# Performance work log

Measured on AMD Instinct MI355X. Metric: run time of the kernel, lower is better.

Reference implementation:

```python
import jax, jax.numpy as jnp
import numpy as np

N = 400000      # total atoms
MAXD = 4        # max degree
NDEG = MAXD + 1 # degrees 0..4 (DeepChem min_degree=0)
F0 = 75         # ConvMolFeaturizer atom feature size
B = 16384       # number of graphs (batch_size)
NT = 12         # n_tasks
DIMS = [F0, 15, 20, 27, 36]


def setup_inputs() -> dict:
    key = jax.random.key(0)
    ks = jax.random.split(key, 40)
    inp = {}
    inp["atom_features"] = jax.random.normal(ks[0], (N, F0), jnp.float32)
    i = 1
    for l in range(4):
        fi, fo = DIMS[l], DIMS[l + 1]
        inp[f"Ws{l+1}"] = jax.random.normal(ks[i], (NDEG, fi, fo), jnp.float32) * 0.1; i += 1
        inp[f"Wn{l+1}"] = jax.random.normal(ks[i], (NDEG, fi, fo), jnp.float32) * 0.1; i += 1
        inp[f"b{l+1}"] = jax.random.normal(ks[i], (NDEG, fo), jnp.float32) * 0.1; i += 1
    inp["Wd2"] = jax.random.normal(ks[i], (2 * DIMS[-1], NT * 2), jnp.float32) * 0.1; i += 1
    inp["bd2"] = jnp.zeros((NT * 2,), jnp.float32)
    inp["Wl1"] = jax.random.normal(ks[i], (2 * NT, 96), jnp.float32) * 0.1; i += 1
    inp["bl1"] = jnp.zeros((96,), jnp.float32)
    inp["g1"] = jnp.ones((96,), jnp.float32)
    inp["be1"] = jnp.zeros((96,), jnp.float32)
    inp["Wl2"] = jax.random.normal(ks[i], (96, 63), jnp.float32) * 0.1; i += 1
    inp["bl2"] = jnp.zeros((63,), jnp.float32)
    inp["g2"] = jnp.ones((63,), jnp.float32)
    inp["be2"] = jnp.zeros((63,), jnp.float32)
    inp["Wl3"] = jax.random.normal(ks[i], (63, 138), jnp.float32) * 0.1; i += 1
    inp["bl3"] = jnp.zeros((138,), jnp.float32)
    inp["neighbor_list"] = jax.random.randint(ks[i], (N, MAXD), 0, N, dtype=jnp.int32); i += 1
    inp["degree"] = jax.random.randint(ks[i], (N,), 0, NDEG, dtype=jnp.int32); i += 1
    inp["membership"] = jnp.sort(jax.random.randint(ks[i], (N,), 0, B, dtype=jnp.int32)); i += 1
    inp["batch_size"] = B
    return inp


def _graph_conv(x, Ws, Wn, b, nbr, deg_onehot, nmask):
    # gather neighbor features and sum over (masked) neighbor slots: [N, Fin]
    nsum = (x[nbr] * nmask).sum(axis=1)
    # per-degree affine (DeepChem: separate self/neighbor weights per degree)
    pre = (jnp.einsum('nf,dfg->ndg', x, Ws)
           + jnp.einsum('nf,dfg->ndg', nsum, Wn)
           + b[None])                              # [N, NDEG, Fout]
    out = jnp.einsum('nd,ndg->ng', deg_onehot, pre)  # select row for atom's degree
    return jax.nn.selu(out)


def _bn(x, g, b, eps=1e-5):
    m = x.mean(axis=0)
    v = x.var(axis=0)
    return (x - m) * jax.lax.rsqrt(v + eps) * g + b


def reference(atom_features, Ws1, Wn1, b1, Ws2, Wn2, b2, Ws3, Wn3, b3,
              Ws4, Wn4, b4, Wd2, bd2, Wl1, bl1, g1, be1,
              Wl2, bl2, g2, be2, Wl3, bl3,
              neighbor_list, degree, membership, batch_size):
    deg_onehot = jax.nn.one_hot(degree, NDEG, dtype=atom_features.dtype)
    nmask = (jnp.arange(MAXD, dtype=degree.dtype)[None, :] < degree[:, None])
    nmask = nmask.astype(atom_features.dtype)[:, :, None]          # [N, MAXD, 1]

    x = _graph_conv(atom_features, Ws1, Wn1, b1, neighbor_list, deg_onehot, nmask)
    x = _graph_conv(x, Ws2, Wn2, b2, neighbor_list, deg_onehot, nmask)
    x = _graph_conv(x, Ws3, Wn3, b3, neighbor_list, deg_onehot, nmask)
    x = _graph_conv(x, Ws4, Wn4, b4, neighbor_list, deg_onehot, nmask)

    # GraphGather readout: concat(segment_sum, segment_max) then selu
    s = jax.ops.segment_sum(x, membership, num_segments=batch_size,
                            indices_are_sorted=True)
    m = jax.ops.segment_max(x, membership, num_segments=batch_size,
                            indices_are_sorted=True)
    m = jnp.where(jnp.isfinite(m), m, 0.0)  # empty graphs -> 0
    r = jax.nn.selu(jnp.concatenate([s, m], axis=1))               # [B, 72]

    logits = (r @ Wd2 + bd2).reshape(batch_size, -1, 2)            # [B, NT, 2]
    p = jax.nn.softmax(logits, axis=-1).reshape(batch_size, -1)    # [B, 2*NT]

    h = jax.nn.relu(_bn(p @ Wl1 + bl1, g1, be1))
    h = jax.nn.relu(_bn(h @ Wl2 + bl2, g2, be2))
    return jax.nn.sigmoid(h @ Wl3 + bl3)                            # [B, 138]
```

## Files before the change

### kernel.cpp

```cpp
#include <hip/hip_runtime.h>
#include <hip/hip_bf16.h>

#define N_ATOMS 400000
#define MAX_D   4
#define NDEG_   5
#define B_GR    16384
#define NTASK   12
#define AT      256
#define PADCAP  401408

__device__ __forceinline__ float selu_f(float x) {
    const float a = 1.6732632423543772f, s = 1.0507009873554805f;
    return x > 0.f ? s * x : s * a * (__expf(x) - 1.f);
}

__global__ void zero_kernel(int* ctr) {
    if (threadIdx.x < 10) ctr[threadIdx.x] = 0;
}

__launch_bounds__(256)
__global__ void fill_kernel(int* idx, int* degs_s) {
    const int e = blockIdx.x * 256 + threadIdx.x;
    if (e < PADCAP) { idx[e] = -1; degs_s[e] = -1; }
}

__launch_bounds__(256)
__global__ void hist_kernel(const int* __restrict__ deg, int* ctr) {
    __shared__ int h[NDEG_];
    if (threadIdx.x < NDEG_) h[threadIdx.x] = 0;
    __syncthreads();
    for (int i = blockIdx.x * 256 + threadIdx.x; i < N_ATOMS; i += gridDim.x * 256)
        atomicAdd(&h[deg[i]], 1);
    __syncthreads();
    if (threadIdx.x < NDEG_ && h[threadIdx.x]) atomicAdd(&ctr[threadIdx.x], h[threadIdx.x]);
}

__global__ void offsets_kernel(int* ctr) {
    if (threadIdx.x == 0) {
        int run = 0;
        for (int d = 0; d < NDEG_; ++d) {
            ctr[10 + d] = run;
            run += ctr[d];
            run = (run + AT - 1) & ~(AT - 1);
        }
        ctr[15] = run;
    }
}

__launch_bounds__(256)
__global__ void scatter_kernel(const int* __restrict__ deg, int* ctr,
                               int* idx, int* rank, int* degs_s) {
    __shared__ int h[NDEG_];
    __shared__ int base[NDEG_];
    const int i = blockIdx.x * 256 + threadIdx.x;
    const int d = (i < N_ATOMS) ? deg[i] : -1;
    if (threadIdx.x < NDEG_) h[threadIdx.x] = 0;
    __syncthreads();
    int intra = 0;
    if (i < N_ATOMS) intra = atomicAdd(&h[d], 1);
    __syncthreads();
    if (threadIdx.x < NDEG_ && h[threadIdx.x] > 0)
        base[threadIdx.x] = atomicAdd(&ctr[5 + threadIdx.x], h[threadIdx.x]);
    __syncthreads();
    if (i < N_ATOMS) {
        const int p = ctr[10 + d] + base[d] + intra;
        idx[p] = i;
        rank[i] = p;
        degs_s[p] = d;
    }
}

__launch_bounds__(256)
__global__ void nbrprep_kernel(const int* __restrict__ nbr, const int* __restrict__ rank,
                               int4* __restrict__ nbrs_s, int4* __restrict__ nbro_s) {
    const int i = blockIdx.x * 256 + threadIdx.x;
    if (i >= N_ATOMS) return;
    const int p = rank[i];
    const int4 nb = *reinterpret_cast<const int4*>(nbr + (size_t)i * MAX_D);
    nbro_s[p] = nb;
    nbrs_s[p] = make_int4(rank[nb.x], rank[nb.y], rank[nb.z], rank[nb.w]);
}

template<int FI, int FIP, int FO, bool FIRST, bool SCATTER_OUT>
__launch_bounds__(256)
__global__ void conv_fused2(const float* __restrict__ x,
                            const int4*  __restrict__ nbr_,
                            const float* __restrict__ Ws,
                            const float* __restrict__ Wn,
                            const float* __restrict__ bias,
                            const int*   __restrict__ degs_s,
                            const int*   __restrict__ idx,
                            float*       __restrict__ outs)
{
    __shared__ float xt[64][FIP];
    __shared__ float nt[64][FIP];
    __shared__ int   s_a[64];
    __shared__ int   s_d[64];
    __shared__ int4  s_nb[64];

    const int pb = blockIdx.x * 64;
    const int dfirst = degs_s[pb];
    if (dfirst < 0) return;
    const int tid = threadIdx.x;

    if (tid < 64) {
        const int p = pb + tid;
        int a = FIRST ? idx[p] : p;
        s_a[tid] = (a < 0) ? 0 : a;
        s_d[tid] = degs_s[p];
        s_nb[tid] = nbr_[p];
    }
    __syncthreads();

    for (int e = tid; e < 64 * FI; e += 256) {
        const int al = e / FI, f = e - al * FI;
        const int d = s_d[al];
        xt[al][f] = x[(size_t)s_a[al] * FI + f];
        float s = 0.f;
        if (d > 0) {
            const int4 nb = s_nb[al];
            s += x[(size_t)nb.x * FI + f];
            if (d > 1) s += x[(size_t)nb.y * FI + f];
            if (d > 2) s += x[(size_t)nb.z * FI + f];
            if (d > 3) s += x[(size_t)nb.w * FI + f];
        }
        nt[al][f] = s;
    }
    __syncthreads();

    if (tid < 64) {
        const int d = __builtin_amdgcn_readfirstlane(dfirst);
        const float* __restrict__ wsd = Ws + d * FI * FO;
        const float* __restrict__ wnd = Wn + d * FI * FO;
        const float* __restrict__ bb  = bias + d * FO;

        float acc[FO];
        #pragma unroll
        for (int o = 0; o < FO; ++o) acc[o] = bb[o];

        for (int f = 0; f < FI; ++f) {
            const float xv = xt[tid][f];
            const float nv = nt[tid][f];
            const float* __restrict__ wsf = wsd + f * FO;
            const float* __restrict__ wnf = wnd + f * FO;
            #pragma unroll
            for (int o = 0; o < FO; ++o)
                acc[o] = fmaf(xv, wsf[o], fmaf(nv, wnf[o], acc[o]));
        }

        int row; bool store;
        if (SCATTER_OUT) { row = idx[pb + tid]; store = (row >= 0); }
        else             { row = pb + tid;      store = true; }
        if (store) {
            float* __restrict__ orow = outs + (size_t)row * FO;
            #pragma unroll
            for (int o = 0; o < FO; ++o) orow[o] = selu_f(acc[o]);
        }
    }
}

__launch_bounds__(64)
__global__ void readout_kernel(const float* __restrict__ x4o,
                               const int*   __restrict__ mem,
                               const float* __restrict__ Wd2,
                               const float* __restrict__ bd2,
                               float*       __restrict__ p)
{
    const int g = blockIdx.x;
    const int t = threadIdx.x;

    int lo = 0, hi = N_ATOMS;
    while (lo < hi) { int mid = (lo + hi) >> 1; if (mem[mid] < g) lo = mid + 1; else hi = mid; }
    int lo2 = lo, hi2 = N_ATOMS;
    while (lo2 < hi2) { int mid = (lo2 + hi2) >> 1; if (mem[mid] < g + 1) lo2 = mid + 1; else hi2 = mid; }

    __shared__ float r[72];
    if (t < 36) {
        float s = 0.f, m = -3.4e38f;
        for (int a = lo; a < lo2; ++a) {
            float v = x4o[(size_t)a * 36 + t];
            s += v;
            m = fmaxf(m, v);
        }
        if (lo2 == lo) m = 0.f;
        r[t]      = selu_f(s);
        r[36 + t] = selu_f(m);
    }
    __syncthreads();
    if (t < 24) {
        float acc = bd2[t];
        #pragma unroll
        for (int f = 0; f < 72; ++f) acc += r[f] * Wd2[f * 24 + t];
        float part = __shfl_xor(acc, 1);
        p[g * 24 + t] = 1.f / (1.f + __expf(part - acc));
    }
}

__launch_bounds__(256)
__global__ void dense1_kernel(const float* __restrict__ p,
                              const float* __restrict__ Wl1,
                              const float* __restrict__ bl1,
                              float*       __restrict__ y1)
{
    const int idx = blockIdx.x * 256 + threadIdx.x;
    if (idx >= B_GR * 96) return;
    const int row = idx / 96, c = idx - row * 96;
    float acc = bl1[c];
    const float* pr = p + row * 24;
    #pragma unroll
    for (int f = 0; f < 24; ++f) acc += pr[f] * Wl1[f * 96 + c];
    y1[idx] = acc;
}

template<int C>
__launch_bounds__(256)
__global__ void stats_kernel(const float* __restrict__ y, float* __restrict__ st)
{
    const int c = blockIdx.x;
    float s = 0.f, q = 0.f;
    for (int r = threadIdx.x; r < B_GR; r += 256) {
        const float v = y[r * C + c];
        s += v; q += v * v;
    }
    __shared__ float ss[256], qq[256];
    ss[threadIdx.x] = s; qq[threadIdx.x] = q;
    __syncthreads();
    for (int off = 128; off > 0; off >>= 1) {
        if (threadIdx.x < off) {
            ss[threadIdx.x] += ss[threadIdx.x + off];
            qq[threadIdx.x] += qq[threadIdx.x + off];
        }
        __syncthreads();
    }
    if (threadIdx.x == 0) {
        const float mean = ss[0] / (float)B_GR;
        const float var  = qq[0] / (float)B_GR - mean * mean;
        st[c]     = mean;
        st[C + c] = rsqrtf(var + 1e-5f);
    }
}

__launch_bounds__(256)
__global__ void dense2_kernel(const float* __restrict__ y1,
                              const float* __restrict__ st1,
                              const float* __restrict__ g1,
                              const float* __restrict__ be1,
                              const float* __restrict__ Wl2,
                              const float* __restrict__ bl2,
                              float*       __restrict__ y2)
{
    __shared__ float h[4 * 96];
    const int r0 = blockIdx.x * 4;
    for (int e = threadIdx.x; e < 4 * 96; e += 256) {
        const int rr = e / 96, c = e - rr * 96;
        float v = y1[(r0 + rr) * 96 + c];
        v = (v - st1[c]) * st1[96 + c] * g1[c] + be1[c];
        h[e] = fmaxf(v, 0.f);
    }
    __syncthreads();
    for (int e = threadIdx.x; e < 4 * 63; e += 256) {
        const int rr = e / 63, o = e - rr * 63;
        float acc = bl2[o];
        #pragma unroll
        for (int f = 0; f < 96; ++f) acc += h[rr * 96 + f] * Wl2[f * 63 + o];
        y2[(r0 + rr) * 63 + o] = acc;
    }
}

__launch_bounds__(320)
__global__ void dense3_kernel(const float* __restrict__ y2,
                              const float* __restrict__ st2,
                              const float* __restrict__ g2,
                              const float* __restrict__ be2,
                              const float* __restrict__ Wl3,
                              const float* __restrict__ bl3,
                              float*       __restrict__ out)
{
    __shared__ float h[2 * 63];
    const int r0 = blockIdx.x * 2;
    for (int e = threadIdx.x; e < 2 * 63; e += 320) {
        const int rr = e / 63, c = e - rr * 63;
        float v = y2[(r0 + rr) * 63 + c];
        v = (v - st2[c]) * st2[63 + c] * g2[c] + be2[c];
        h[e] = fmaxf(v, 0.f);
    }
    __syncthreads();
    for (int e = threadIdx.x; e < 2 * 138; e += 320) {
        const int rr = e / 138, o = e - rr * 138;
        float acc = bl3[o];
        #pragma unroll
        for (int f = 0; f < 63; ++f) acc += h[rr * 63 + f] * Wl3[f * 138 + o];
        out[(r0 + rr) * 138 + o] = 1.f / (1.f + __expf(-acc));
    }
}

extern "C" void kernel_launch(void* const* d_in, const int* in_sizes, int n_in,
                              void* d_out, int out_size, void* d_ws, size_t ws_size,
                              hipStream_t stream)
{
    (void)in_sizes; (void)n_in; (void)out_size; (void)ws_size;

    const float* af  = (const float*)d_in[0];
    const float* Ws1 = (const float*)d_in[1];
    const float* Wn1 = (const float*)d_in[2];
    const float* b1  = (const float*)d_in[3];
    const float* Ws2 = (const float*)d_in[4];
    const float* Wn2 = (const float*)d_in[5];
    const float* b2  = (const float*)d_in[6];
    const float* Ws3 = (const float*)d_in[7];
    const float* Wn3 = (const float*)d_in[8];
    const float* b3  = (const float*)d_in[9];
    const float* Ws4 = (const float*)d_in[10];
    const float* Wn4 = (const float*)d_in[11];
    const float* b4  = (const float*)d_in[12];
    const float* Wd2 = (const float*)d_in[13];
    const float* bd2 = (const float*)d_in[14];
    const float* Wl1 = (const float*)d_in[15];
    const float* bl1 = (const float*)d_in[16];
    const float* g1  = (const float*)d_in[17];
    const float* be1 = (const float*)d_in[18];
    const float* Wl2 = (const float*)d_in[19];
    const float* bl2 = (const float*)d_in[20];
    const float* g2  = (const float*)d_in[21];
    const float* be2 = (const float*)d_in[22];
    const float* Wl3 = (const float*)d_in[23];
    const float* bl3 = (const float*)d_in[24];
    const int*   nbr = (const int*)d_in[25];
    const int*   deg = (const int*)d_in[26];
    const int*   mem = (const int*)d_in[27];

    float* ws = (float*)d_ws;
    float* A = ws;
    float* B = A + (size_t)PADCAP * 27;
    int*   idx    = (int*)(B + (size_t)PADCAP * 36);
    int*   rank   = idx + PADCAP;
    int*   degs_s = rank + N_ATOMS;
    int4*  nbrs_s = (int4*)(degs_s + PADCAP);
    int4*  nbro_s = nbrs_s + PADCAP;
    int*   ctr    = (int*)(nbro_s + PADCAP);

    float* x1  = A;
    float* x2  = B;
    float* x3  = A;
    float* x4o = B;
    float* p   = A;
    float* y1  = A + 393216;
    float* y2  = A + 393216 + 1572864;
    float* st1 = A + 393216 + 1572864 + 1032192;
    float* st2 = st1 + 192;

    zero_kernel<<<1, 16, 0, stream>>>(ctr);
    fill_kernel<<<PADCAP / 256, 256, 0, stream>>>(idx, degs_s);
    hist_kernel<<<1024, 256, 0, stream>>>(deg, ctr);
    offsets_kernel<<<1, 1, 0, stream>>>(ctr);
    scatter_kernel<<<(N_ATOMS + 255) / 256, 256, 0, stream>>>(deg, ctr, idx, rank, degs_s);
    nbrprep_kernel<<<(N_ATOMS + 255) / 256, 256, 0, stream>>>(nbr, rank, nbrs_s, nbro_s);

    conv_fused2<75, 77, 15, true,  false><<<PADCAP / 64, 256, 0, stream>>>
        (af, nbro_s, Ws1, Wn1, b1, degs_s, idx, x1);
    conv_fused2<15, 17, 20, false, false><<<PADCAP / 64, 256, 0, stream>>>
        (x1, nbrs_s, Ws2, Wn2, b2, degs_s, idx, x2);
    conv_fused2<20, 21, 27, false, false><<<PADCAP / 64, 256, 0, stream>>>
        (x2, nbrs_s, Ws3, Wn3, b3, degs_s, idx, x3);
    conv_fused2<27, 29, 36, false, true ><<<PADCAP / 64, 256, 0, stream>>>
        (x3, nbrs_s, Ws4, Wn4, b4, degs_s, idx, x4o);

    readout_kernel<<<B_GR, 64, 0, stream>>>(x4o, mem, Wd2, bd2, p);

    dense1_kernel<<<(B_GR * 96) / 256, 256, 0, stream>>>(p, Wl1, bl1, y1);
    stats_kernel<96><<<96, 256, 0, stream>>>(y1, st1);
    dense2_kernel<<<B_GR / 4, 256, 0, stream>>>(y1, st1, g1, be1, Wl2, bl2, y2);
    stats_kernel<63><<<63, 256, 0, stream>>>(y2, st2);
    dense3_kernel<<<B_GR / 2, 320, 0, stream>>>(y2, st2, g2, be2, Wl3, bl3, (float*)d_out);
}
```

Baseline: 804.9 us.

## Split conv output features across four waves and halve atom tile

The graph-conv kernel now uses 32-atom tiles instead of 64, and the compute phase is spread over all four wavefronts. Each wave computes a quarter of the output features, where before a single wave computed all of them while three sat idle. This aims to use the whole block for the FMA work and to double the number of blocks, improving latency hiding. In exchange, each block does less gather work, half of each wave's lanes are idle, and the guarded output columns can leave some lanes doing nothing useful.

```diff
diff --git a/kernel.cpp b/kernel.cpp
--- a/kernel.cpp
+++ b/kernel.cpp
@@ -7,6 +7,7 @@
 #define B_GR    16384
 #define NTASK   12
 #define AT      256
+#define TA      32
 #define PADCAP  401408
 
 __device__ __forceinline__ float selu_f(float x) {
@@ -83,7 +84,7 @@
 
 template<int FI, int FIP, int FO, bool FIRST, bool SCATTER_OUT>
 __launch_bounds__(256)
-__global__ void conv_fused2(const float* __restrict__ x,
+__global__ void conv_fused3(const float* __restrict__ x,
                             const int4*  __restrict__ nbr_,
                             const float* __restrict__ Ws,
                             const float* __restrict__ Wn,
@@ -92,18 +93,18 @@
                             const int*   __restrict__ idx,
                             float*       __restrict__ outs)
 {
-    __shared__ float xt[64][FIP];
-    __shared__ float nt[64][FIP];
-    __shared__ int   s_a[64];
-    __shared__ int   s_d[64];
-    __shared__ int4  s_nb[64];
-
-    const int pb = blockIdx.x * 64;
+    __shared__ float xt[TA][FIP];
+    __shared__ float nt[TA][FIP];
+    __shared__ int   s_a[TA];
+    __shared__ int   s_d[TA];
+    __shared__ int4  s_nb[TA];
+
+    const int pb = blockIdx.x * TA;
     const int dfirst = degs_s[pb];
     if (dfirst < 0) return;
     const int tid = threadIdx.x;
 
-    if (tid < 64) {
+    if (tid < TA) {
         const int p = pb + tid;
         int a = FIRST ? idx[p] : p;
         s_a[tid] = (a < 0) ? 0 : a;
@@ -112,7 +113,7 @@
     }
     __syncthreads();
 
-    for (int e = tid; e < 64 * FI; e += 256) {
+    for (int e = tid; e < TA * FI; e += 256) {
         const int al = e / FI, f = e - al * FI;
         const int d = s_d[al];
         xt[al][f] = x[(size_t)s_a[al] * FI + f];
@@ -128,33 +129,42 @@
     }
     __syncthreads();
 
-    if (tid < 64) {
+    const int w = tid >> 6;
+    const int l = tid & 63;
+    if (l < TA) {
+        constexpr int OPG = (FO + 3) / 4;
+        const int o0 = w * OPG;
+        const int al = l;
         const int d = __builtin_amdgcn_readfirstlane(dfirst);
-        const float* __restrict__ wsd = Ws + d * FI * FO;
-        const float* __restrict__ wnd = Wn + d * FI * FO;
-        const float* __restrict__ bb  = bias + d * FO;
-
-        float acc[FO];
+        const float* __restrict__ wsd = Ws + (d * FI) * FO + o0;
+        const float* __restrict__ wnd = Wn + (d * FI) * FO + o0;
+        const float* __restrict__ bb  = bias + d * FO + o0;
+
+        float acc[OPG];
         #pragma unroll
-        for (int o = 0; o < FO; ++o) acc[o] = bb[o];
+        for (int oo = 0; oo < OPG; ++oo)
+            acc[oo] = (o0 + oo < FO) ? bb[oo] : 0.f;
 
         for (int f = 0; f < FI; ++f) {
-            const float xv = xt[tid][f];
-            const float nv = nt[tid][f];
+            const float xv = xt[al][f];
+            const float nv = nt[al][f];
             const float* __restrict__ wsf = wsd + f * FO;
             const float* __restrict__ wnf = wnd + f * FO;
             #pragma unroll
-            for (int o = 0; o < FO; ++o)
-                acc[o] = fmaf(xv, wsf[o], fmaf(nv, wnf[o], acc[o]));
+            for (int oo = 0; oo < OPG; ++oo) {
+                if (o0 + oo < FO)
+                    acc[oo] = fmaf(xv, wsf[oo], fmaf(nv, wnf[oo], acc[oo]));
+            }
         }
 
         int row; bool store;
-        if (SCATTER_OUT) { row = idx[pb + tid]; store = (row >= 0); }
-        else             { row = pb + tid;      store = true; }
+        if (SCATTER_OUT) { row = idx[pb + al]; store = (row >= 0); }
+        else             { row = pb + al;      store = true; }
         if (store) {
-            float* __restrict__ orow = outs + (size_t)row * FO;
+            float* __restrict__ orow = outs + (size_t)row * FO + o0;
             #pragma unroll
-            for (int o = 0; o < FO; ++o) orow[o] = selu_f(acc[o]);
+            for (int oo = 0; oo < OPG; ++oo)
+                if (o0 + oo < FO) orow[oo] = selu_f(acc[oo]);
         }
     }
 }
@@ -356,13 +366,13 @@
     scatter_kernel<<<(N_ATOMS + 255) / 256, 256, 0, stream>>>(deg, ctr, idx, rank, degs_s);
     nbrprep_kernel<<<(N_ATOMS + 255) / 256, 256, 0, stream>>>(nbr, rank, nbrs_s, nbro_s);
 
-    conv_fused2<75, 77, 15, true,  false><<<PADCAP / 64, 256, 0, stream>>>
+    conv_fused3<75, 77, 15, true,  false><<<PADCAP / TA, 256, 0, stream>>>
         (af, nbro_s, Ws1, Wn1, b1, degs_s, idx, x1);
-    conv_fused2<15, 17, 20, false, false><<<PADCAP / 64, 256, 0, stream>>>
+    conv_fused3<15, 17, 20, false, false><<<PADCAP / TA, 256, 0, stream>>>
         (x1, nbrs_s, Ws2, Wn2, b2, degs_s, idx, x2);
-    conv_fused2<20, 21, 27, false, false><<<PADCAP / 64, 256, 0, stream>>>
+    conv_fused3<20, 21, 27, false, false><<<PADCAP / TA, 256, 0, stream>>>
         (x2, nbrs_s, Ws3, Wn3, b3, degs_s, idx, x3);
-    conv_fused2<27, 29, 36, false, true ><<<PADCAP / 64, 256, 0, stream>>>
+    conv_fused3<27, 29, 36, false, true ><<<PADCAP / TA, 256, 0, stream>>>
         (x3, nbrs_s, Ws4, Wn4, b4, degs_s, idx, x4o);
 
     readout_kernel<<<B_GR, 64, 0, stream>>>(x4o, mem, Wd2, bd2, p);
```

After: 1.322 ms. 64.2% more time.
